# Kernel tuning notes

Hardware: AMD Instinct MI355X
Metric: run time of the kernel (lower is better)

## Reference

```python
import jax, jax.numpy as jnp
import numpy as np


def setup_inputs() -> dict:
    key = jax.random.key(0)
    ks = jax.random.split(key, 6)
    B, L, D, H, U = 256, 225, 1280, 256, 256
    features = jax.random.normal(ks[0], (B, L, D), dtype=jnp.float32)
    hidden = jax.random.normal(ks[1], (B, H), dtype=jnp.float32)
    W1 = jax.random.normal(ks[2], (D, U), dtype=jnp.float32) * (1.0 / np.sqrt(D))
    b1 = jnp.zeros((U,), dtype=jnp.float32)
    W2 = jax.random.normal(ks[3], (H, U), dtype=jnp.float32) * (1.0 / np.sqrt(H))
    b2 = jnp.zeros((U,), dtype=jnp.float32)
    V = jax.random.normal(ks[4], (U, 1), dtype=jnp.float32) * (1.0 / np.sqrt(U))
    bV = jnp.zeros((1,), dtype=jnp.float32)
    return {"features": features, "hidden": hidden, "W1": W1, "b1": b1,
            "W2": W2, "b2": b2, "V": V, "bV": bV}


def reference(features, hidden, W1, b1, W2, b2, V, bV):
    # features: [B, L, D]; hidden: [B, H]
    proj_f = jnp.einsum('bld,du->blu', features, W1) + b1        # [B, L, U]
    proj_h = (hidden @ W2 + b2)[:, None, :]                      # [B, 1, U]
    score = jnp.tanh(proj_f + proj_h)                            # [B, L, U]
    logits = jnp.einsum('blu,uo->blo', score, V) + bV            # [B, L, 1]
    attn = jax.nn.softmax(logits, axis=1)                        # [B, L, 1]
    context = jnp.sum(attn * features, axis=1)                   # [B, D]
    return context
```

## Files before the change

kernel.cpp:

```cpp
#include <hip/hip_runtime.h>
#include <hip/hip_bf16.h>

#define B_ 256
#define L_ 225
#define D_ 1280
#define H_ 256
#define U_ 256

typedef __bf16  bf16x8 __attribute__((ext_vector_type(8)));
typedef float   f32x4  __attribute__((ext_vector_type(4)));
typedef unsigned short u16x8 __attribute__((ext_vector_type(8)));
typedef unsigned short u16x4 __attribute__((ext_vector_type(4)));

__device__ __forceinline__ unsigned short f2bf(float f) {
    union { __hip_bfloat16 h; unsigned short u; } cv;
    cv.h = __float2bfloat16(f);
    return cv.u;
}

__device__ __forceinline__ f32x4 bf4_to_f32(u16x4 w) {
    union { unsigned u; float f; } a0, a1, a2, a3;
    a0.u = (unsigned)w[0] << 16; a1.u = (unsigned)w[1] << 16;
    a2.u = (unsigned)w[2] << 16; a3.u = (unsigned)w[3] << 16;
    return (f32x4){a0.f, a1.f, a2.f, a3.f};
}

__device__ __forceinline__ void gload_lds16(const void* g, void* l) {
    __builtin_amdgcn_global_load_lds(
        (const __attribute__((address_space(1))) unsigned int*)g,
        (__attribute__((address_space(3))) unsigned int*)l,
        16, 0, 0);
}

__device__ __forceinline__ float wredsum(float x) {
#pragma unroll
    for (int off = 32; off > 0; off >>= 1) x += __shfl_xor(x, off, 64);
    return x;
}

__global__ void k_prep_w1t(const float* __restrict__ W1, __hip_bfloat16* __restrict__ w1t) {
    int idx = blockIdx.x * 256 + threadIdx.x;
    int k = idx / U_;
    int u = idx % U_;
    w1t[(size_t)u * D_ + k] = __float2bfloat16(W1[idx]);
}

__global__ void k_proj_h(const float* __restrict__ hidden, const float* __restrict__ W2,
                         const float* __restrict__ b1, const float* __restrict__ b2,
                         float* __restrict__ ph) {
    __shared__ float sh[H_];
    int b = blockIdx.x;
    int u = threadIdx.x;
    sh[u] = hidden[b * H_ + u];
    __syncthreads();
    float acc = b1[u] + b2[u];
#pragma unroll 8
    for (int h = 0; h < H_; ++h) acc += sh[h] * W2[h * U_ + u];
    ph[b * U_ + u] = acc;
}

__global__ __launch_bounds__(1024) void __attribute__((noinline)) k_dummy() {}

template<int BF16WS>
__global__ __launch_bounds__(1024) void k_fused(
        const float* __restrict__ feat,
        const __hip_bfloat16* __restrict__ w1t,
        const float* __restrict__ ph,
        const float* __restrict__ Vv,
        __hip_bfloat16* __restrict__ fbf,
        float* __restrict__ out) {
    __shared__ __align__(128) char smem[138304];
    float* sV   = (float*)(smem + 131072);
    float* sPh  = (float*)(smem + 132096);
    float* sL   = (float*)(smem + 133120);
    float* sW   = (float*)(smem + 137216);
    float* sRed = (float*)(smem + 138240);

    const int tid  = threadIdx.x;
    const int lane = tid & 63;
    const int wave = tid >> 6;
    const int wr   = wave >> 2;
    const int wc   = wave & 3;
    const int b    = blockIdx.x;

    if (tid < 256) { sV[tid] = Vv[tid]; sPh[tid] = ph[b * 256 + tid]; }

    const int ar    = tid >> 2;
    const int arc   = ar < L_ ? ar : (L_ - 1);
    const int akseg = (tid & 3) << 4;
    const float* aSrc0 = feat + ((size_t)(b * L_ + arc) * D_ + akseg);
    __hip_bfloat16* fDst0 = fbf + ((size_t)(b * L_ + arc) * D_ + akseg);
    const int ac80 = akseg >> 3;
    const int aswz = (ar & 7) << 4;

    f32x4 acc[4][4];
#pragma unroll
    for (int mi = 0; mi < 4; ++mi)
#pragma unroll
        for (int ni = 0; ni < 4; ++ni)
            acc[mi][ni] = (f32x4){0.f, 0.f, 0.f, 0.f};

    auto loadA = [&](int kt, f32x4* v) {
        const float* src = aSrc0 + kt * 64;
        v[0] = *reinterpret_cast<const f32x4*>(src);
        v[1] = *reinterpret_cast<const f32x4*>(src + 4);
        v[2] = *reinterpret_cast<const f32x4*>(src + 8);
        v[3] = *reinterpret_cast<const f32x4*>(src + 12);
    };
    auto stageB = [&](int kt, char* bufB) {
#pragma unroll
        for (int pass = 0; pass < 2; ++pass) {
            int s   = pass * 1024 + tid;
            int u   = s >> 3;
            int c8s = s & 7;
            int c8g = c8s ^ (u & 7);
            gload_lds16(w1t + (size_t)u * D_ + kt * 64 + c8g * 8, bufB + s * 16);
        }
    };
    auto storeA = [&](int kt, const f32x4* v, char* bufA) {
        u16x8 w0, w1;
        w0[0] = f2bf(v[0][0]); w0[1] = f2bf(v[0][1]); w0[2] = f2bf(v[0][2]); w0[3] = f2bf(v[0][3]);
        w0[4] = f2bf(v[1][0]); w0[5] = f2bf(v[1][1]); w0[6] = f2bf(v[1][2]); w0[7] = f2bf(v[1][3]);
        w1[0] = f2bf(v[2][0]); w1[1] = f2bf(v[2][1]); w1[2] = f2bf(v[2][2]); w1[3] = f2bf(v[2][3]);
        w1[4] = f2bf(v[3][0]); w1[5] = f2bf(v[3][1]); w1[6] = f2bf(v[3][2]); w1[7] = f2bf(v[3][3]);
        *reinterpret_cast<u16x8*>(bufA + (ar << 7) + ((ac80 << 4) ^ aswz))       = w0;
        *reinterpret_cast<u16x8*>(bufA + (ar << 7) + (((ac80 + 1) << 4) ^ aswz)) = w1;
        if (BF16WS && ar < L_) {
            *reinterpret_cast<u16x8*>(fDst0 + kt * 64)     = w0;
            *reinterpret_cast<u16x8*>(fDst0 + kt * 64 + 8) = w1;
        }
    };
    auto compute = [&](const char* bufA, const char* bufB) {
#pragma unroll
        for (int ks = 0; ks < 2; ++ks) {
            const int kk2 = (ks * 32 + ((lane >> 4) << 3)) * 2;
            bf16x8 a[4], bb[4];
#pragma unroll
            for (int mi = 0; mi < 4; ++mi) {
                int r = wr * 64 + mi * 16 + (lane & 15);
                a[mi] = *reinterpret_cast<const bf16x8*>(bufA + (r << 7) + (kk2 ^ ((r & 7) << 4)));
            }
#pragma unroll
            for (int ni = 0; ni < 4; ++ni) {
                int u = wc * 64 + ni * 16 + (lane & 15);
                bb[ni] = *reinterpret_cast<const bf16x8*>(bufB + (u << 7) + (kk2 ^ ((u & 7) << 4)));
            }
#pragma unroll
            for (int mi = 0; mi < 4; ++mi)
#pragma unroll
                for (int ni = 0; ni < 4; ++ni)
                    acc[mi][ni] = __builtin_amdgcn_mfma_f32_16x16x32_bf16(
                        a[mi], bb[ni], acc[mi][ni], 0, 0, 0);
        }
    };

    {
        f32x4 v[4];
        loadA(0, v);
        stageB(0, smem + 32768);
        storeA(0, v, smem);
    }
    __syncthreads();
    int cur = 0;
    for (int kt = 0; kt < 20; ++kt) {
        char* bufN = smem + (cur ^ 1) * 65536;
        f32x4 v[4];
        if (kt < 19) { loadA(kt + 1, v); stageB(kt + 1, bufN + 32768); }
        char* bufC = smem + cur * 65536;
        compute(bufC, bufC + 32768);
        if (kt < 19) storeA(kt + 1, v, bufN);
        __syncthreads();
        cur ^= 1;
    }

    float phu[4], vu[4];
#pragma unroll
    for (int ni = 0; ni < 4; ++ni) {
        int u = wc * 64 + ni * 16 + (lane & 15);
        phu[ni] = sPh[u];
        vu[ni]  = sV[u];
    }
#pragma unroll
    for (int mi = 0; mi < 4; ++mi) {
#pragma unroll
        for (int rg = 0; rg < 4; ++rg) {
            int row = wr * 64 + mi * 16 + ((lane >> 4) << 2) + rg;
            float s = 0.f;
#pragma unroll
            for (int ni = 0; ni < 4; ++ni) {
                float x = acc[mi][ni][rg] + phu[ni];
                s += (1.f - 2.f / (__expf(2.f * x) + 1.f)) * vu[ni];
            }
            s += __shfl_xor(s, 1, 64);
            s += __shfl_xor(s, 2, 64);
            s += __shfl_xor(s, 4, 64);
            s += __shfl_xor(s, 8, 64);
            if ((lane & 15) == 0) sL[wc * 256 + row] = s;
        }
    }
    __syncthreads();
    float den_p = 0.f;
    if (tid < 256) {
        float lg = sL[tid] + sL[256 + tid] + sL[512 + tid] + sL[768 + tid];
        float w  = (tid < L_) ? __expf(lg) : 0.f;
        sW[tid] = w;
        den_p = w;
    }
    den_p = wredsum(den_p);
    if (lane == 0) sRed[wave] = den_p;
    __syncthreads();

    f32x4 c[5];
#pragma unroll
    for (int ch = 0; ch < 5; ++ch) c[ch] = (f32x4){0.f, 0.f, 0.f, 0.f};

    if (BF16WS) {
        const char* fB = (const char*)(fbf + (size_t)b * L_ * D_);
        int l = wave;
        for (; l + 16 < L_; l += 32) {
            float wa = sW[l], wb = sW[l + 16];
            const char* ra = fB + (size_t)l * 2560;
            const char* rb = fB + (size_t)(l + 16) * 2560;
            u16x8 a0 = *reinterpret_cast<const u16x8*>(ra + lane * 16);
            u16x8 a1 = *reinterpret_cast<const u16x8*>(ra + 1024 + lane * 16);
            u16x4 a2 = *reinterpret_cast<const u16x4*>(ra + 2048 + lane * 8);
            u16x8 b0 = *reinterpret_cast<const u16x8*>(rb + lane * 16);
            u16x8 b1 = *reinterpret_cast<const u16x8*>(rb + 1024 + lane * 16);
            u16x4 b2 = *reinterpret_cast<const u16x4*>(rb + 2048 + lane * 8);
            c[0] += wa * bf4_to_f32((u16x4){a0[0],a0[1],a0[2],a0[3]});
            c[1] += wa * bf4_to_f32((u16x4){a0[4],a0[5],a0[6],a0[7]});
            c[2] += wa * bf4_to_f32((u16x4){a1[0],a1[1],a1[2],a1[3]});
            c[3] += wa * bf4_to_f32((u16x4){a1[4],a1[5],a1[6],a1[7]});
            c[4] += wa * bf4_to_f32(a2);
            c[0] += wb * bf4_to_f32((u16x4){b0[0],b0[1],b0[2],b0[3]});
            c[1] += wb * bf4_to_f32((u16x4){b0[4],b0[5],b0[6],b0[7]});
            c[2] += wb * bf4_to_f32((u16x4){b1[0],b1[1],b1[2],b1[3]});
            c[3] += wb * bf4_to_f32((u16x4){b1[4],b1[5],b1[6],b1[7]});
            c[4] += wb * bf4_to_f32(b2);
        }
        if (l < L_) {
            float wa = sW[l];
            const char* ra = fB + (size_t)l * 2560;
            u16x8 a0 = *reinterpret_cast<const u16x8*>(ra + lane * 16);
            u16x8 a1 = *reinterpret_cast<const u16x8*>(ra + 1024 + lane * 16);
            u16x4 a2 = *reinterpret_cast<const u16x4*>(ra + 2048 + lane * 8);
            c[0] += wa * bf4_to_f32((u16x4){a0[0],a0[1],a0[2],a0[3]});
            c[1] += wa * bf4_to_f32((u16x4){a0[4],a0[5],a0[6],a0[7]});
            c[2] += wa * bf4_to_f32((u16x4){a1[0],a1[1],a1[2],a1[3]});
            c[3] += wa * bf4_to_f32((u16x4){a1[4],a1[5],a1[6],a1[7]});
            c[4] += wa * bf4_to_f32(a2);
        }
    } else {
        const float* fB = feat + (size_t)b * L_ * D_;
        int l = wave;
        for (; l + 16 < L_; l += 32) {
            float wa = sW[l], wb = sW[l + 16];
            const float* ra = fB + (size_t)l * D_ + (lane << 2);
            const float* rb = fB + (size_t)(l + 16) * D_ + (lane << 2);
#pragma unroll
            for (int ch = 0; ch < 5; ++ch) {
                c[ch] += wa * *reinterpret_cast<const f32x4*>(ra + ch * 256);
                c[ch] += wb * *reinterpret_cast<const f32x4*>(rb + ch * 256);
            }
        }
        if (l < L_) {
            float wa = sW[l];
            const float* ra = fB + (size_t)l * D_ + (lane << 2);
#pragma unroll
            for (int ch = 0; ch < 5; ++ch)
                c[ch] += wa * *reinterpret_cast<const f32x4*>(ra + ch * 256);
        }
    }

    float* pc = (float*)smem;
    if (BF16WS) {
#pragma unroll
        for (int ch = 0; ch < 4; ++ch)
            *reinterpret_cast<f32x4*>(pc + wave * 1280 + (ch >> 1) * 512 + lane * 8 + (ch & 1) * 4) = c[ch];
        *reinterpret_cast<f32x4*>(pc + wave * 1280 + 1024 + lane * 4) = c[4];
    } else {
#pragma unroll
        for (int ch = 0; ch < 5; ++ch)
            *reinterpret_cast<f32x4*>(pc + wave * 1280 + ch * 256 + (lane << 2)) = c[ch];
    }
    __syncthreads();
    if (tid < 320) {
        f32x4 s = (f32x4){0.f, 0.f, 0.f, 0.f};
#pragma unroll
        for (int w = 0; w < 16; ++w)
            s += *reinterpret_cast<const f32x4*>(pc + w * 1280 + (tid << 2));
        float den = 0.f;
#pragma unroll
        for (int i = 0; i < 16; ++i) den += sRed[i];
        s *= (1.f / den);
        *reinterpret_cast<f32x4*>(out + (size_t)b * D_ + (tid << 2)) = s;
    }
}

extern "C" void kernel_launch(void* const* d_in, const int* in_sizes, int n_in,
                              void* d_out, int out_size, void* d_ws, size_t ws_size,
                              hipStream_t stream) {
    const float* feat   = (const float*)d_in[0];
    const float* hidden = (const float*)d_in[1];
    const float* W1     = (const float*)d_in[2];
    const float* b1     = (const float*)d_in[3];
    const float* W2     = (const float*)d_in[4];
    const float* b2     = (const float*)d_in[5];
    const float* Vv     = (const float*)d_in[6];

    char* ws = (char*)d_ws;
    __hip_bfloat16* w1t = (__hip_bfloat16*)(ws);
    float* ph           = (float*)(ws + 655360);
    __hip_bfloat16* fbf = (__hip_bfloat16*)(ws + 917504);
    float* out = (float*)d_out;

    const size_t need = 917504ull + (size_t)B_ * L_ * D_ * 2ull;

    k_prep_w1t<<<(U_ * D_) / 256, 256, 0, stream>>>(W1, w1t);
    k_proj_h  <<<B_, U_, 0, stream>>>(hidden, W2, b1, b2, ph);
    if (ws_size >= need)
        k_fused<1><<<B_, 1024, 0, stream>>>(feat, w1t, ph, Vv, fbf, out);
    else
        k_fused<0><<<B_, 1024, 0, stream>>>(feat, w1t, ph, Vv, fbf, out);
}
```

Baseline: 146.7 us.

## Drop bf16 feature workspace copy and merge prep kernels into one launch

Removes the path that wrote a bf16 copy of the features to workspace during the GEMM and read it back for the context sum. The context pass now re-reads the fp32 features directly. The two small prep kernels (W1 transpose and hidden projection) are merged into a single launch, and launch_bounds gains a min-blocks hint of 4. This trades the extra bf16 writes for twice-as-large fp32 reads in the weighted sum, and saves one kernel launch.

```diff
diff --git a/kernel.cpp b/kernel.cpp
--- a/kernel.cpp
+++ b/kernel.cpp
@@ -10,19 +10,11 @@
 typedef __bf16  bf16x8 __attribute__((ext_vector_type(8)));
 typedef float   f32x4  __attribute__((ext_vector_type(4)));
 typedef unsigned short u16x8 __attribute__((ext_vector_type(8)));
-typedef unsigned short u16x4 __attribute__((ext_vector_type(4)));
 
 __device__ __forceinline__ unsigned short f2bf(float f) {
     union { __hip_bfloat16 h; unsigned short u; } cv;
     cv.h = __float2bfloat16(f);
     return cv.u;
-}
-
-__device__ __forceinline__ f32x4 bf4_to_f32(u16x4 w) {
-    union { unsigned u; float f; } a0, a1, a2, a3;
-    a0.u = (unsigned)w[0] << 16; a1.u = (unsigned)w[1] << 16;
-    a2.u = (unsigned)w[2] << 16; a3.u = (unsigned)w[3] << 16;
-    return (f32x4){a0.f, a1.f, a2.f, a3.f};
 }
 
 __device__ __forceinline__ void gload_lds16(const void* g, void* l) {
@@ -38,36 +30,37 @@
     return x;
 }
 
-__global__ void k_prep_w1t(const float* __restrict__ W1, __hip_bfloat16* __restrict__ w1t) {
-    int idx = blockIdx.x * 256 + threadIdx.x;
-    int k = idx / U_;
-    int u = idx % U_;
-    w1t[(size_t)u * D_ + k] = __float2bfloat16(W1[idx]);
-}
-
-__global__ void k_proj_h(const float* __restrict__ hidden, const float* __restrict__ W2,
-                         const float* __restrict__ b1, const float* __restrict__ b2,
-                         float* __restrict__ ph) {
-    __shared__ float sh[H_];
-    int b = blockIdx.x;
-    int u = threadIdx.x;
-    sh[u] = hidden[b * H_ + u];
-    __syncthreads();
-    float acc = b1[u] + b2[u];
+__global__ void k_prep(const float* __restrict__ W1,
+                       const float* __restrict__ hidden,
+                       const float* __restrict__ W2,
+                       const float* __restrict__ b1,
+                       const float* __restrict__ b2,
+                       __hip_bfloat16* __restrict__ w1t,
+                       float* __restrict__ ph) {
+    int bid = blockIdx.x;
+    if (bid < 1280) {
+        int idx = bid * 256 + threadIdx.x;
+        int k = idx / U_;
+        int u = idx % U_;
+        w1t[(size_t)u * D_ + k] = __float2bfloat16(W1[idx]);
+    } else {
+        __shared__ float sh[H_];
+        int b = bid - 1280;
+        int u = threadIdx.x;
+        sh[u] = hidden[b * H_ + u];
+        __syncthreads();
+        float acc = b1[u] + b2[u];
 #pragma unroll 8
-    for (int h = 0; h < H_; ++h) acc += sh[h] * W2[h * U_ + u];
-    ph[b * U_ + u] = acc;
-}
-
-__global__ __launch_bounds__(1024) void __attribute__((noinline)) k_dummy() {}
-
-template<int BF16WS>
-__global__ __launch_bounds__(1024) void k_fused(
+        for (int h = 0; h < H_; ++h) acc += sh[h] * W2[h * U_ + u];
+        ph[b * U_ + u] = acc;
+    }
+}
+
+__global__ __launch_bounds__(1024, 4) void k_fused(
         const float* __restrict__ feat,
         const __hip_bfloat16* __restrict__ w1t,
         const float* __restrict__ ph,
         const float* __restrict__ Vv,
-        __hip_bfloat16* __restrict__ fbf,
         float* __restrict__ out) {
     __shared__ __align__(128) char smem[138304];
     float* sV   = (float*)(smem + 131072);
@@ -89,7 +82,6 @@
     const int arc   = ar < L_ ? ar : (L_ - 1);
     const int akseg = (tid & 3) << 4;
     const float* aSrc0 = feat + ((size_t)(b * L_ + arc) * D_ + akseg);
-    __hip_bfloat16* fDst0 = fbf + ((size_t)(b * L_ + arc) * D_ + akseg);
     const int ac80 = akseg >> 3;
     const int aswz = (ar & 7) << 4;
 
@@ -117,7 +109,7 @@
             gload_lds16(w1t + (size_t)u * D_ + kt * 64 + c8g * 8, bufB + s * 16);
         }
     };
-    auto storeA = [&](int kt, const f32x4* v, char* bufA) {
+    auto storeA = [&](const f32x4* v, char* bufA) {
         u16x8 w0, w1;
         w0[0] = f2bf(v[0][0]); w0[1] = f2bf(v[0][1]); w0[2] = f2bf(v[0][2]); w0[3] = f2bf(v[0][3]);
         w0[4] = f2bf(v[1][0]); w0[5] = f2bf(v[1][1]); w0[6] = f2bf(v[1][2]); w0[7] = f2bf(v[1][3]);
@@ -125,10 +117,6 @@
         w1[4] = f2bf(v[3][0]); w1[5] = f2bf(v[3][1]); w1[6] = f2bf(v[3][2]); w1[7] = f2bf(v[3][3]);
         *reinterpret_cast<u16x8*>(bufA + (ar << 7) + ((ac80 << 4) ^ aswz))       = w0;
         *reinterpret_cast<u16x8*>(bufA + (ar << 7) + (((ac80 + 1) << 4) ^ aswz)) = w1;
-        if (BF16WS && ar < L_) {
-            *reinterpret_cast<u16x8*>(fDst0 + kt * 64)     = w0;
-            *reinterpret_cast<u16x8*>(fDst0 + kt * 64 + 8) = w1;
-        }
     };
     auto compute = [&](const char* bufA, const char* bufB) {
 #pragma unroll
@@ -158,7 +146,7 @@
         f32x4 v[4];
         loadA(0, v);
         stageB(0, smem + 32768);
-        storeA(0, v, smem);
+        storeA(v, smem);
     }
     __syncthreads();
     int cur = 0;
@@ -168,7 +156,7 @@
         if (kt < 19) { loadA(kt + 1, v); stageB(kt + 1, bufN + 32768); }
         char* bufC = smem + cur * 65536;
         compute(bufC, bufC + 32768);
-        if (kt < 19) storeA(kt + 1, v, bufN);
+        if (kt < 19) storeA(v, bufN);
         __syncthreads();
         cur ^= 1;
     }
@@ -213,44 +201,7 @@
     f32x4 c[5];
 #pragma unroll
     for (int ch = 0; ch < 5; ++ch) c[ch] = (f32x4){0.f, 0.f, 0.f, 0.f};
-
-    if (BF16WS) {
-        const char* fB = (const char*)(fbf + (size_t)b * L_ * D_);
-        int l = wave;
-        for (; l + 16 < L_; l += 32) {
-            float wa = sW[l], wb = sW[l + 16];
-            const char* ra = fB + (size_t)l * 2560;
-            const char* rb = fB + (size_t)(l + 16) * 2560;
-            u16x8 a0 = *reinterpret_cast<const u16x8*>(ra + lane * 16);
-            u16x8 a1 = *reinterpret_cast<const u16x8*>(ra + 1024 + lane * 16);
-            u16x4 a2 = *reinterpret_cast<const u16x4*>(ra + 2048 + lane * 8);
-            u16x8 b0 = *reinterpret_cast<const u16x8*>(rb + lane * 16);
-            u16x8 b1 = *reinterpret_cast<const u16x8*>(rb + 1024 + lane * 16);
-            u16x4 b2 = *reinterpret_cast<const u16x4*>(rb + 2048 + lane * 8);
-            c[0] += wa * bf4_to_f32((u16x4){a0[0],a0[1],a0[2],a0[3]});
-            c[1] += wa * bf4_to_f32((u16x4){a0[4],a0[5],a0[6],a0[7]});
-            c[2] += wa * bf4_to_f32((u16x4){a1[0],a1[1],a1[2],a1[3]});
-            c[3] += wa * bf4_to_f32((u16x4){a1[4],a1[5],a1[6],a1[7]});
-            c[4] += wa * bf4_to_f32(a2);
-            c[0] += wb * bf4_to_f32((u16x4){b0[0],b0[1],b0[2],b0[3]});
-            c[1] += wb * bf4_to_f32((u16x4){b0[4],b0[5],b0[6],b0[7]});
-            c[2] += wb * bf4_to_f32((u16x4){b1[0],b1[1],b1[2],b1[3]});
-            c[3] += wb * bf4_to_f32((u16x4){b1[4],b1[5],b1[6],b1[7]});
-            c[4] += wb * bf4_to_f32(b2);
-        }
-        if (l < L_) {
-            float wa = sW[l];
-            const char* ra = fB + (size_t)l * 2560;
-            u16x8 a0 = *reinterpret_cast<const u16x8*>(ra + lane * 16);
-            u16x8 a1 = *reinterpret_cast<const u16x8*>(ra + 1024 + lane * 16);
-            u16x4 a2 = *reinterpret_cast<const u16x4*>(ra + 2048 + lane * 8);
-            c[0] += wa * bf4_to_f32((u16x4){a0[0],a0[1],a0[2],a0[3]});
-            c[1] += wa * bf4_to_f32((u16x4){a0[4],a0[5],a0[6],a0[7]});
-            c[2] += wa * bf4_to_f32((u16x4){a1[0],a1[1],a1[2],a1[3]});
-            c[3] += wa * bf4_to_f32((u16x4){a1[4],a1[5],a1[6],a1[7]});
-            c[4] += wa * bf4_to_f32(a2);
-        }
-    } else {
+    {
         const float* fB = feat + (size_t)b * L_ * D_;
         int l = wave;
         for (; l + 16 < L_; l += 32) {
@@ -273,16 +224,9 @@
     }
 
     float* pc = (float*)smem;
-    if (BF16WS) {
-#pragma unroll
-        for (int ch = 0; ch < 4; ++ch)
-            *reinterpret_cast<f32x4*>(pc + wave * 1280 + (ch >> 1) * 512 + lane * 8 + (ch & 1) * 4) = c[ch];
-        *reinterpret_cast<f32x4*>(pc + wave * 1280 + 1024 + lane * 4) = c[4];
-    } else {
-#pragma unroll
-        for (int ch = 0; ch < 5; ++ch)
-            *reinterpret_cast<f32x4*>(pc + wave * 1280 + ch * 256 + (lane << 2)) = c[ch];
-    }
+#pragma unroll
+    for (int ch = 0; ch < 5; ++ch)
+        *reinterpret_cast<f32x4*>(pc + wave * 1280 + ch * 256 + (lane << 2)) = c[ch];
     __syncthreads();
     if (tid < 320) {
         f32x4 s = (f32x4){0.f, 0.f, 0.f, 0.f};
@@ -310,16 +254,9 @@
 
     char* ws = (char*)d_ws;
     __hip_bfloat16* w1t = (__hip_bfloat16*)(ws);
-    float* ph           = (float*)(ws + 655360);
-    __hip_bfloat16* fbf = (__hip_bfloat16*)(ws + 917504);
+    float* ph = (float*)(ws + 655360);
     float* out = (float*)d_out;
 
-    const size_t need = 917504ull + (size_t)B_ * L_ * D_ * 2ull;
-
-    k_prep_w1t<<<(U_ * D_) / 256, 256, 0, stream>>>(W1, w1t);
-    k_proj_h  <<<B_, U_, 0, stream>>>(hidden, W2, b1, b2, ph);
-    if (ws_size >= need)
-        k_fused<1><<<B_, 1024, 0, stream>>>(feat, w1t, ph, Vv, fbf, out);
-    else
-        k_fused<0><<<B_, 1024, 0, stream>>>(feat, w1t, ph, Vv, fbf, out);
-}
+    k_prep <<<1536, 256, 0, stream>>>(W1, hidden, W2, b1, b2, w1t, ph);
+    k_fused<<<B_, 1024, 0, stream>>>(feat, w1t, ph, Vv, out);
+}
```

Result: faster. 127.5 us (-13.1%).
